# Performance work log

Hardware: AMD Instinct MI355X
Metric: run time of the kernel (lower is better)

The kernel has to match this reference:

```python
import jax, jax.numpy as jnp
import numpy as np

D, H, DH, DF = 128, 8, 16, 512
N_Q, N_KV, E = 20000, 20000, 640000


def _xavier(key, shape):
    fan_in, fan_out = shape[1], shape[0]
    lim = float(np.sqrt(6.0 / (fan_in + fan_out)))
    return jax.random.uniform(key, shape, jnp.float32, -lim, lim)


def layer_norm(x, g, b, eps=1e-5):
    mu = jnp.mean(x, axis=-1, keepdims=True)
    var = jnp.var(x, axis=-1, keepdims=True)
    return (x - mu) * jax.lax.rsqrt(var + eps) * g + b


def setup_inputs() -> dict:
    key = jax.random.key(0)
    ks = jax.random.split(key, 12)
    return {
        "q_feat": jax.random.normal(ks[0], (N_Q, D), jnp.float32),
        "kv_feat": jax.random.normal(ks[1], (N_KV, D), jnp.float32),
        "src": jax.random.randint(ks[2], (E,), 0, N_KV, jnp.int32),
        "dst": jax.random.randint(ks[3], (E,), 0, N_Q, jnp.int32),
        "Wq": _xavier(ks[4], (H * DH, D)),
        "Wk": _xavier(ks[5], (H * DH, D)),
        "Wv": _xavier(ks[6], (H * DH, D)),
        "Wo": _xavier(ks[7], (D, H * DH)),
        "W1": _xavier(ks[8], (DF, D)),
        "bf1": jnp.zeros((DF,), jnp.float32),
        "W2": _xavier(ks[9], (D, DF)),
        "bf2": jnp.zeros((D,), jnp.float32),
        "ln1_g": jnp.ones((D,), jnp.float32),
        "ln1_b": jnp.zeros((D,), jnp.float32),
        "ln2_g": jnp.ones((D,), jnp.float32),
        "ln2_b": jnp.zeros((D,), jnp.float32),
    }


def reference(q_feat, kv_feat, src, dst, Wq, Wk, Wv, Wo, W1, bf1, W2, bf2,
              ln1_g, ln1_b, ln2_g, ln2_b):
    n_q = q_feat.shape[0]
    # projections -> [N, H, DH]
    q = (q_feat @ Wq.T).reshape(-1, H, DH)
    k = (kv_feat @ Wk.T).reshape(-1, H, DH)
    v = (kv_feat @ Wv.T).reshape(-1, H, DH)
    # edge scores: u_mul_v then sum over d_head, scaled (score per edge per head)
    score = jnp.einsum('ehd,ehd->eh', k[src], q[dst]) / np.sqrt(DH)
    # edge_softmax grouped by destination node
    mx = jax.ops.segment_max(score, dst, num_segments=n_q)  # [Nq, H]
    ex = jnp.exp(score - mx[dst])
    denom = jax.ops.segment_sum(ex, dst, num_segments=n_q)
    att = ex / denom[dst]  # [E, H]
    # weighted scatter-sum of values to destination nodes
    msg = v[src] * att[:, :, None]  # [E, H, DH]
    out = jax.ops.segment_sum(msg, dst, num_segments=n_q)  # [Nq, H, DH]
    sa = out.reshape(n_q, H * DH) @ Wo.T
    feat = layer_norm(q_feat + sa, ln1_g, ln1_b)
    ff = jax.nn.relu(feat @ W1.T + bf1) @ W2.T + bf2
    return layer_norm(feat + ff, ln2_g, ln2_b)
```

## Files before the change

kernel.cpp:

```cpp
#include <hip/hip_runtime.h>
#include <hip/hip_fp16.h>
#include <math.h>
#include <type_traits>

#define D 128
#define NH 8
#define DHD 16
#define DF 512
#define STR 128

typedef _Float16 half8 __attribute__((ext_vector_type(8)));
typedef _Float16 half4 __attribute__((ext_vector_type(4)));
typedef float f32x4 __attribute__((ext_vector_type(4)));


__global__ __launch_bounds__(256) void mega_kernel(
    const float* __restrict__ q_feat, const float* __restrict__ kv_feat,
    const float* __restrict__ Wq, const float* __restrict__ Wk,
    const float* __restrict__ Wv,
    __half* __restrict__ fq, __half* __restrict__ fkv, int NQ, int NKV,
    const int* __restrict__ dst, const int* __restrict__ src,
    int* __restrict__ cnt, int* __restrict__ srcg, int E,
    const float* __restrict__ Wo, const float* __restrict__ W1,
    const float* __restrict__ W2,
    __half* __restrict__ wo16, __half* __restrict__ w116, __half* __restrict__ w216) {
    __shared__ __align__(16) __half As[128 * 128];
    __shared__ __align__(16) __half Ws[64 * 128];

    int xt = blockIdx.x;
    int tid = threadIdx.x;

    if (xt >= 2) {
        if (xt == 18) {
            int g = blockIdx.y * 256 + tid;
            if (g < 36864) {
                const float* s;
                __half* d;
                int idx = g;
                if (idx < 4096) { s = Wo; d = wo16; }
                else if (idx < 20480) { idx -= 4096; s = W1; d = w116; }
                else { idx -= 20480; s = W2; d = w216; }
                float4 f = ((const float4*)s)[idx];
                ushort4 o;
                o.x = __half_as_ushort(__float2half(f.x));
                o.y = __half_as_ushort(__float2half(f.y));
                o.z = __half_as_ushort(__float2half(f.z));
                o.w = __half_as_ushort(__float2half(f.w));
                ((ushort4*)d)[idx] = o;
            }
            return;
        }
        int b = (xt - 2) * gridDim.y + blockIdx.y;
        int i = b * 256 + tid;
        if (i < E) {
            int dn = dst[i];
            int p = atomicAdd(&cnt[dn], 1);
            if (p < STR) srcg[((size_t)dn << 7) + p] = src[i];
        }
        return;
    }

    const float* A = xt ? kv_feat : q_feat;
    __half* C = xt ? fkv : fq;
    int O = xt ? 256 : 128;
    int NCT = xt ? 4 : 2;
    int N = xt ? NKV : NQ;
    int row0 = blockIdx.y * 128;
    if (row0 >= N) return;

    int lane = tid & 63;
    int w = tid >> 6;
    int wm = w >> 1, wn = w & 1;
    int l16 = lane & 15, lq = lane >> 4;

#pragma unroll
    for (int i = 0; i < 8; ++i) {
        int f = tid + i * 256;
        int ln = f & 63;
        int mt = (f >> 6) & 7;
        int kc = f >> 9;
        int m = row0 + mt * 16 + (ln & 15);
        int k = kc * 32 + (ln >> 4) * 8;
        half8 v = {};
        if (m < N) {
            const float4* p = (const float4*)(A + (size_t)m * 128 + k);
            float4 f0 = p[0], f1 = p[1];
            v = (half8){(_Float16)f0.x, (_Float16)f0.y, (_Float16)f0.z, (_Float16)f0.w,
                        (_Float16)f1.x, (_Float16)f1.y, (_Float16)f1.z, (_Float16)f1.w};
        }
        ((half8*)As)[f] = v;
    }

    for (int ct = 0; ct < NCT; ++ct) {
        __syncthreads();
#pragma unroll
        for (int i = 0; i < 4; ++i) {
            int f = tid + i * 256;
            int ln = f & 63;
            int nt = (f >> 6) & 3;
            int kc = f >> 8;
            int n = ct * 64 + nt * 16 + (ln & 15);
            int k = kc * 32 + (ln >> 4) * 8;
            const float* Wsrc;
            int r;
            if (xt == 0) {
                Wsrc = Wq; r = n;
            } else {
                int h = n >> 5, qd = (n >> 3) & 3, isv = (n >> 2) & 1, d2 = n & 3;
                r = h * 16 + qd * 4 + d2;
                Wsrc = isv ? Wv : Wk;
            }
            const float4* p = (const float4*)(Wsrc + (size_t)r * 128 + k);
            float4 f0 = p[0], f1 = p[1];
            ((half8*)Ws)[f] = (half8){(_Float16)f0.x, (_Float16)f0.y, (_Float16)f0.z, (_Float16)f0.w,
                                      (_Float16)f1.x, (_Float16)f1.y, (_Float16)f1.z, (_Float16)f1.w};
        }
        __syncthreads();
        f32x4 acc[4][2];
#pragma unroll
        for (int i = 0; i < 4; ++i)
#pragma unroll
            for (int j = 0; j < 2; ++j) acc[i][j] = (f32x4){0.f, 0.f, 0.f, 0.f};
#pragma unroll
        for (int kc = 0; kc < 4; ++kc) {
            half8 a[4], b[2];
#pragma unroll
            for (int i = 0; i < 4; ++i) a[i] = ((half8*)As)[(kc * 8 + wm * 4 + i) * 64 + lane];
#pragma unroll
            for (int j = 0; j < 2; ++j) b[j] = ((half8*)Ws)[(kc * 4 + wn * 2 + j) * 64 + lane];
#pragma unroll
            for (int i = 0; i < 4; ++i)
#pragma unroll
                for (int j = 0; j < 2; ++j)
                    acc[i][j] = __builtin_amdgcn_mfma_f32_16x16x32_f16(a[i], b[j], acc[i][j], 0, 0, 0);
        }
#pragma unroll
        for (int i = 0; i < 4; ++i) {
            int rbase = row0 + (wm * 4 + i) * 16 + lq * 4;
#pragma unroll
            for (int j = 0; j < 2; ++j) {
                int c = ct * 64 + (wn * 2 + j) * 16 + l16;
#pragma unroll
                for (int r = 0; r < 4; ++r) {
                    int row = rbase + r;
                    if (row < N) C[(size_t)row * O + c] = __float2half(acc[i][j][r]);
                }
            }
        }
    }
}


__global__ __launch_bounds__(256) void attn_kernel(
    const __half* __restrict__ q, const __half* __restrict__ kv,
    const int* __restrict__ srcg, const int* __restrict__ cnt,
    __half* __restrict__ out, int NQ) {
    int n = blockIdx.x * 4 + (threadIdx.x >> 6);
    if (n >= NQ) return;
    int lane = threadIdx.x & 63;
    int eh = lane >> 5;
    int sub = lane & 31;
    int doff = sub << 2;
    half4 q4 = *(const half4*)(q + (size_t)n * D + doff);
    float q0 = (float)q4[0] * 0.25f, q1 = (float)q4[1] * 0.25f;
    float q2 = (float)q4[2] * 0.25f, q3 = (float)q4[3] * 0.25f;
    int s0 = n << 7;
    int c_ = cnt[n];
    int s1 = s0 + (c_ < STR ? c_ : STR);
    float lA = 0.f, lB = 0.f, lC = 0.f, lD = 0.f;
    f32x4 aA = {0.f, 0.f, 0.f, 0.f}, aB = {0.f, 0.f, 0.f, 0.f};
    f32x4 aC = {0.f, 0.f, 0.f, 0.f}, aD = {0.f, 0.f, 0.f, 0.f};
    int j = s0;
    for (; j + 8 <= s1; j += 8) {
        int e0 = srcg[j + eh];
        int e1 = srcg[j + 2 + eh];
        int e2 = srcg[j + 4 + eh];
        int e3 = srcg[j + 6 + eh];
        half8 c0 = *(const half8*)(kv + (size_t)e0 * 256 + (sub << 3));
        half8 c1 = *(const half8*)(kv + (size_t)e1 * 256 + (sub << 3));
        half8 c2 = *(const half8*)(kv + (size_t)e2 * 256 + (sub << 3));
        half8 c3 = *(const half8*)(kv + (size_t)e3 * 256 + (sub << 3));
        float p0 = q0 * (float)c0[0] + q1 * (float)c0[1] + q2 * (float)c0[2] + q3 * (float)c0[3];
        float p1 = q0 * (float)c1[0] + q1 * (float)c1[1] + q2 * (float)c1[2] + q3 * (float)c1[3];
        float p2 = q0 * (float)c2[0] + q1 * (float)c2[1] + q2 * (float)c2[2] + q3 * (float)c2[3];
        float p3 = q0 * (float)c3[0] + q1 * (float)c3[1] + q2 * (float)c3[2] + q3 * (float)c3[3];
        p0 += __shfl_xor(p0, 1, 4); p0 += __shfl_xor(p0, 2, 4);
        p1 += __shfl_xor(p1, 1, 4); p1 += __shfl_xor(p1, 2, 4);
        p2 += __shfl_xor(p2, 1, 4); p2 += __shfl_xor(p2, 2, 4);
        p3 += __shfl_xor(p3, 1, 4); p3 += __shfl_xor(p3, 2, 4);
        float x0 = __expf(fminf(p0, 70.f));
        float x1 = __expf(fminf(p1, 70.f));
        float x2 = __expf(fminf(p2, 70.f));
        float x3 = __expf(fminf(p3, 70.f));
        lA += x0; lB += x1; lC += x2; lD += x3;
        aA[0] += x0 * (float)c0[4]; aA[1] += x0 * (float)c0[5];
        aA[2] += x0 * (float)c0[6]; aA[3] += x0 * (float)c0[7];
        aB[0] += x1 * (float)c1[4]; aB[1] += x1 * (float)c1[5];
        aB[2] += x1 * (float)c1[6]; aB[3] += x1 * (float)c1[7];
        aC[0] += x2 * (float)c2[4]; aC[1] += x2 * (float)c2[5];
        aC[2] += x2 * (float)c2[6]; aC[3] += x2 * (float)c2[7];
        aD[0] += x3 * (float)c3[4]; aD[1] += x3 * (float)c3[5];
        aD[2] += x3 * (float)c3[6]; aD[3] += x3 * (float)c3[7];
    }
    for (; j + 4 <= s1; j += 4) {
        int e0 = srcg[j + eh];
        int e1 = srcg[j + 2 + eh];
        half8 c0 = *(const half8*)(kv + (size_t)e0 * 256 + (sub << 3));
        half8 c1 = *(const half8*)(kv + (size_t)e1 * 256 + (sub << 3));
        float p0 = q0 * (float)c0[0] + q1 * (float)c0[1] + q2 * (float)c0[2] + q3 * (float)c0[3];
        float p1 = q0 * (float)c1[0] + q1 * (float)c1[1] + q2 * (float)c1[2] + q3 * (float)c1[3];
        p0 += __shfl_xor(p0, 1, 4); p0 += __shfl_xor(p0, 2, 4);
        p1 += __shfl_xor(p1, 1, 4); p1 += __shfl_xor(p1, 2, 4);
        float x0 = __expf(fminf(p0, 70.f));
        float x1 = __expf(fminf(p1, 70.f));
        lA += x0; lB += x1;
        aA[0] += x0 * (float)c0[4]; aA[1] += x0 * (float)c0[5];
        aA[2] += x0 * (float)c0[6]; aA[3] += x0 * (float)c0[7];
        aB[0] += x1 * (float)c1[4]; aB[1] += x1 * (float)c1[5];
        aB[2] += x1 * (float)c1[6]; aB[3] += x1 * (float)c1[7];
    }
    for (; j < s1; j += 2) {
        bool valid = (j + eh) < s1;
        int e0 = srcg[valid ? (j + eh) : s0];
        half8 c0 = *(const half8*)(kv + (size_t)e0 * 256 + (sub << 3));
        float p0 = q0 * (float)c0[0] + q1 * (float)c0[1] + q2 * (float)c0[2] + q3 * (float)c0[3];
        p0 += __shfl_xor(p0, 1, 4); p0 += __shfl_xor(p0, 2, 4);
        float x0 = valid ? __expf(fminf(p0, 70.f)) : 0.f;
        lA += x0;
        aA[0] += x0 * (float)c0[4]; aA[1] += x0 * (float)c0[5];
        aA[2] += x0 * (float)c0[6]; aA[3] += x0 * (float)c0[7];
    }
    float l = (lA + lB) + (lC + lD);
    f32x4 a;
#pragma unroll
    for (int i = 0; i < 4; ++i) a[i] = (aA[i] + aB[i]) + (aC[i] + aD[i]);
    l += __shfl_xor(l, 32);
#pragma unroll
    for (int i = 0; i < 4; ++i) a[i] += __shfl_xor(a[i], 32);
    if (eh == 0) {
        float rl = (l > 0.f) ? 1.f / l : 0.f;
        half4 o = {(_Float16)(a[0] * rl), (_Float16)(a[1] * rl),
                   (_Float16)(a[2] * rl), (_Float16)(a[3] * rl)};
        *(half4*)(out + (size_t)n * D + doff) = o;
    }
}


__device__ __forceinline__ int feat_idx64(int rr, int mt, int c) {
    return (((c >> 5) * 4 + mt) * 64 + ((c >> 3) & 3) * 16 + rr) * 8 + (c & 7);
}

__global__ __launch_bounds__(256) void tail_kernel(
    const __half* __restrict__ A , const __half* __restrict__ Wo16,
    const float* __restrict__ res1 ,
    const float* __restrict__ g1, const float* __restrict__ b1,
    const __half* __restrict__ W1h, const float* __restrict__ fb1,
    const __half* __restrict__ W2h, const float* __restrict__ fb2,
    const float* __restrict__ g2, const float* __restrict__ b2,
    float* __restrict__ out, int N) {
    __shared__ __align__(16) __half Feat[64 * 128];
    __shared__ __align__(16) __half S1[64 * 128];
    __shared__ __align__(16) __half S2[128 * 64];
    __shared__ __align__(16) __half Hs[64 * 64];
    int tid = threadIdx.x, lane = tid & 63, w = tid >> 6;
    int row0 = blockIdx.x * 64;
    int l16 = lane & 15, lq = lane >> 4;

#pragma unroll
    for (int i = 0; i < 4; ++i) {
        int f = tid + i * 256;
        int ln = f & 63, mt = (f >> 6) & 3, kc = f >> 8;
        int m = row0 + mt * 16 + (ln & 15);
        int k = kc * 32 + (ln >> 4) * 8;
        half8 av = {};
        if (m < N) av = *(const half8*)(A + (size_t)m * D + k);
        ((half8*)S1)[f] = av;
    }

    f32x4 acc[8];
#pragma unroll
    for (int j = 0; j < 8; ++j) acc[j] = (f32x4){0.f, 0.f, 0.f, 0.f};
#pragma unroll
    for (int kt = 0; kt < 2; ++kt) {
        __syncthreads();
#pragma unroll
        for (int i = 0; i < 4; ++i) {
            int f = tid + i * 256;
            int ln = f & 63, ot = (f >> 6) & 7, kc2 = f >> 9;
            int o = ot * 16 + (ln & 15);
            int k = kt * 64 + kc2 * 32 + (ln >> 4) * 8;
            ((half8*)S2)[f] = *(const half8*)(Wo16 + (size_t)o * D + k);
        }
        __syncthreads();
#pragma unroll
        for (int kc2 = 0; kc2 < 2; ++kc2) {
            half8 a = ((half8*)S1)[((kt * 2 + kc2) * 4 + w) * 64 + lane];
            half8 bf[8];
#pragma unroll
            for (int j = 0; j < 8; ++j) bf[j] = ((half8*)S2)[(kc2 * 8 + j) * 64 + lane];
#pragma unroll
            for (int j = 0; j < 8; ++j)
                acc[j] = __builtin_amdgcn_mfma_f32_16x16x32_f16(a, bf[j], acc[j], 0, 0, 0);
        }
    }
    __syncthreads();

#pragma unroll
    for (int r = 0; r < 4; ++r) {
        int rr = lq * 4 + r;
        int row = row0 + w * 16 + rr;
        bool valid = row < N;
        float vals[8];
        float s = 0.f, sq = 0.f;
#pragma unroll
        for (int j = 0; j < 8; ++j) {
            int c = j * 16 + l16;
            float v = acc[j][r];
            if (valid) v += res1[(size_t)row * D + c];
            vals[j] = v;
            s += v;
            sq += v * v;
        }
#pragma unroll
        for (int m = 1; m < 16; m <<= 1) {
            s += __shfl_xor(s, m, 16);
            sq += __shfl_xor(sq, m, 16);
        }
        float mu = s * (1.f / 128.f);
        float var = sq * (1.f / 128.f) - mu * mu;
        float inv = rsqrtf(var + 1e-5f);
#pragma unroll
        for (int j = 0; j < 8; ++j) {
            int c = j * 16 + l16;
            float o = (vals[j] - mu) * inv * g1[c] + b1[c];
            Feat[feat_idx64(rr, w, c)] = __float2half(o);
        }
    }
    __syncthreads();

    half8 a_all[4];
#pragma unroll
    for (int kc = 0; kc < 4; ++kc)
        a_all[kc] = ((half8*)Feat)[(kc * 4 + w) * 64 + lane];

    f32x4 oacc[8];
#pragma unroll
    for (int j = 0; j < 8; ++j) oacc[j] = (f32x4){0.f, 0.f, 0.f, 0.f};

    for (int hc = 0; hc < 8; ++hc) {
        __syncthreads();
#pragma unroll
        for (int i = 0; i < 4; ++i) {
            int f = tid + i * 256;
            int ln = f & 63, nt = (f >> 6) & 3, kc = f >> 8;
            int n = hc * 64 + nt * 16 + (ln & 15);
            int k = kc * 32 + (ln >> 4) * 8;
            ((half8*)S1)[f] = *(const half8*)(W1h + (size_t)n * D + k);
        }
#pragma unroll
        for (int i = 0; i < 4; ++i) {
            int f = tid + i * 256;
            int ln = f & 63, ot = (f >> 6) & 7, kc2 = f >> 9;
            int o = ot * 16 + (ln & 15);
            int k = hc * 64 + kc2 * 32 + (ln >> 4) * 8;
            ((half8*)S2)[f] = *(const half8*)(W2h + (size_t)o * DF + k);
        }
        __syncthreads();
        f32x4 hacc[4];
#pragma unroll
        for (int j = 0; j < 4; ++j) hacc[j] = (f32x4){0.f, 0.f, 0.f, 0.f};
#pragma unroll
        for (int kc = 0; kc < 4; ++kc) {
            half8 b[4];
#pragma unroll
            for (int j = 0; j < 4; ++j) b[j] = ((half8*)S1)[(kc * 4 + j) * 64 + lane];
#pragma unroll
            for (int j = 0; j < 4; ++j)
                hacc[j] = __builtin_amdgcn_mfma_f32_16x16x32_f16(a_all[kc], b[j], hacc[j], 0, 0, 0);
        }
#pragma unroll
        for (int j = 0; j < 4; ++j) {
            float bias1 = fb1[hc * 64 + j * 16 + l16];
#pragma unroll
            for (int r = 0; r < 4; ++r) {
                float v = fmaxf(hacc[j][r] + bias1, 0.f);
                int kc2 = j >> 1;
                int lanep = ((j & 1) * 2 + (l16 >> 3)) * 16 + lq * 4 + r;
                Hs[((kc2 * 4 + w) * 64 + lanep) * 8 + (l16 & 7)] = __float2half(v);
            }
        }
        __syncthreads();
#pragma unroll
        for (int kc2 = 0; kc2 < 2; ++kc2) {
            half8 a = ((half8*)Hs)[(kc2 * 4 + w) * 64 + lane];
            half8 b[8];
#pragma unroll
            for (int ot = 0; ot < 8; ++ot) b[ot] = ((half8*)S2)[(kc2 * 8 + ot) * 64 + lane];
#pragma unroll
            for (int ot = 0; ot < 8; ++ot)
                oacc[ot] = __builtin_amdgcn_mfma_f32_16x16x32_f16(a, b[ot], oacc[ot], 0, 0, 0);
        }
    }

#pragma unroll
    for (int r = 0; r < 4; ++r) {
        int rr = lq * 4 + r;
        int row = row0 + w * 16 + rr;
        bool valid = row < N;
        float vals[8];
        float s = 0.f, sq = 0.f;
#pragma unroll
        for (int j = 0; j < 8; ++j) {
            int c = j * 16 + l16;
            float v = oacc[j][r] + fb2[c] + __half2float(Feat[feat_idx64(rr, w, c)]);
            vals[j] = v;
            s += v;
            sq += v * v;
        }
#pragma unroll
        for (int m = 1; m < 16; m <<= 1) {
            s += __shfl_xor(s, m, 16);
            sq += __shfl_xor(sq, m, 16);
        }
        float mu = s * (1.f / 128.f);
        float var = sq * (1.f / 128.f) - mu * mu;
        float inv = rsqrtf(var + 1e-5f);
        if (valid) {
#pragma unroll
            for (int j = 0; j < 8; ++j) {
                int c = j * 16 + l16;
                out[(size_t)row * D + c] = (vals[j] - mu) * inv * g2[c] + b2[c];
            }
        }
    }
}


extern "C" void kernel_launch(void* const* d_in, const int* in_sizes, int n_in,
                              void* d_out, int out_size, void* d_ws, size_t ws_size,
                              hipStream_t stream) {
    const float* q_feat = (const float*)d_in[0];
    const float* kv_feat = (const float*)d_in[1];
    const int* src = (const int*)d_in[2];
    const int* dst = (const int*)d_in[3];
    const float* Wq = (const float*)d_in[4];
    const float* Wk = (const float*)d_in[5];
    const float* Wv = (const float*)d_in[6];
    const float* Wo = (const float*)d_in[7];
    const float* W1 = (const float*)d_in[8];
    const float* bf1 = (const float*)d_in[9];
    const float* W2 = (const float*)d_in[10];
    const float* bf2 = (const float*)d_in[11];
    const float* ln1g = (const float*)d_in[12];
    const float* ln1b = (const float*)d_in[13];
    const float* ln2g = (const float*)d_in[14];
    const float* ln2b = (const float*)d_in[15];

    int NQ = in_sizes[0] / D;
    int NKV = in_sizes[1] / D;
    int E = in_sizes[2];
    float* out = (float*)d_out;

    char* base = (char*)d_ws;
    size_t off = 0;
    auto alloc = [&](size_t bytes) -> void* {
        void* p = base + off;
        off += (bytes + 255) & ~(size_t)255;
        return p;
    };
    __half* fq16 = (__half*)alloc((size_t)NQ * D * 2);
    __half* fkv = (__half*)alloc((size_t)NKV * 256 * 2);
    __half* fattn16 = (__half*)alloc((size_t)NQ * D * 2);
    int* cnt = (int*)alloc((size_t)NQ * 4);
    int* srcg = (int*)alloc((size_t)NQ * STR * 4);
    __half* wo16 = (__half*)alloc((size_t)D * D * 2);
    __half* w116 = (__half*)alloc((size_t)DF * D * 2);
    __half* w216 = (__half*)alloc((size_t)D * DF * 2);

    hipMemsetAsync(cnt, 0, (size_t)NQ * sizeof(int), stream);

    dim3 blk(256);
    int NMX = NQ > NKV ? NQ : NKV;
    int ytiles = (NMX + 127) / 128;
    mega_kernel<<<dim3(19, ytiles), blk, 0, stream>>>(
        q_feat, kv_feat, Wq, Wk, Wv, fq16, fkv, NQ, NKV,
        dst, src, cnt, srcg, E, Wo, W1, W2, wo16, w116, w216);

    attn_kernel<<<(NQ + 3) / 4, blk, 0, stream>>>(fq16, fkv, srcg, cnt, fattn16, NQ);

    tail_kernel<<<(NQ + 63) / 64, blk, 0, stream>>>(
        fattn16, wo16, q_feat, ln1g, ln1b, w116, bf1, w216, bf2, ln2g, ln2b, out, NQ);
}
```

Baseline: 215.9 us.

## Shrink projection tiles, vectorize CSR fill, store 16-bit source indices

Narrows the projection GEMM row tile from 128 to 64 rows, with each wave covering 16 rows across all 64 columns. This doubles the block count and halves shared memory per block, aiming for better occupancy. The edge bucketing now handles four edges per thread with int4 loads and stores source indices as 16-bit values, halving the srcg footprint and its traffic. The 16-bit indices assume NKV fits in 65536, and the grid is resized to match.

After: 213.1 us. About the same (-1.3%).

```diff
diff --git a/kernel.cpp b/kernel.cpp
--- a/kernel.cpp
+++ b/kernel.cpp
@@ -20,18 +20,18 @@
     const float* __restrict__ Wv,
     __half* __restrict__ fq, __half* __restrict__ fkv, int NQ, int NKV,
     const int* __restrict__ dst, const int* __restrict__ src,
-    int* __restrict__ cnt, int* __restrict__ srcg, int E,
+    int* __restrict__ cnt, unsigned short* __restrict__ srcg, int E,
     const float* __restrict__ Wo, const float* __restrict__ W1,
     const float* __restrict__ W2,
     __half* __restrict__ wo16, __half* __restrict__ w116, __half* __restrict__ w216) {
-    __shared__ __align__(16) __half As[128 * 128];
+    __shared__ __align__(16) __half As[64 * 128];
     __shared__ __align__(16) __half Ws[64 * 128];
 
     int xt = blockIdx.x;
     int tid = threadIdx.x;
 
     if (xt >= 2) {
-        if (xt == 18) {
+        if (xt == (int)gridDim.x - 1) {
             int g = blockIdx.y * 256 + tid;
             if (g < 36864) {
                 const float* s;
@@ -51,11 +51,28 @@
             return;
         }
         int b = (xt - 2) * gridDim.y + blockIdx.y;
-        int i = b * 256 + tid;
-        if (i < E) {
-            int dn = dst[i];
-            int p = atomicAdd(&cnt[dn], 1);
-            if (p < STR) srcg[((size_t)dn << 7) + p] = src[i];
+        int i4 = b * 256 + tid;
+        int base = i4 << 2;
+        if (base < E) {
+            int dd[4], ss[4];
+            if (base + 3 < E) {
+                int4 d4 = ((const int4*)dst)[i4];
+                int4 s4 = ((const int4*)src)[i4];
+                dd[0] = d4.x; dd[1] = d4.y; dd[2] = d4.z; dd[3] = d4.w;
+                ss[0] = s4.x; ss[1] = s4.y; ss[2] = s4.z; ss[3] = s4.w;
+#pragma unroll
+                for (int u = 0; u < 4; ++u) {
+                    int p = atomicAdd(&cnt[dd[u]], 1);
+                    if (p < STR) srcg[((size_t)dd[u] << 7) + p] = (unsigned short)ss[u];
+                }
+            } else {
+                for (int u = 0; u < 4 && base + u < E; ++u) {
+                    int dn = dst[base + u];
+                    int sn = src[base + u];
+                    int p = atomicAdd(&cnt[dn], 1);
+                    if (p < STR) srcg[((size_t)dn << 7) + p] = (unsigned short)sn;
+                }
+            }
         }
         return;
     }
@@ -65,20 +82,19 @@
     int O = xt ? 256 : 128;
     int NCT = xt ? 4 : 2;
     int N = xt ? NKV : NQ;
-    int row0 = blockIdx.y * 128;
+    int row0 = blockIdx.y * 64;
     if (row0 >= N) return;
 
     int lane = tid & 63;
     int w = tid >> 6;
-    int wm = w >> 1, wn = w & 1;
     int l16 = lane & 15, lq = lane >> 4;
 
 #pragma unroll
-    for (int i = 0; i < 8; ++i) {
+    for (int i = 0; i < 4; ++i) {
         int f = tid + i * 256;
         int ln = f & 63;
-        int mt = (f >> 6) & 7;
-        int kc = f >> 9;
+        int mt = (f >> 6) & 3;
+        int kc = f >> 8;
         int m = row0 + mt * 16 + (ln & 15);
         int k = kc * 32 + (ln >> 4) * 8;
         half8 v = {};
@@ -116,35 +132,26 @@
                                       (_Float16)f1.x, (_Float16)f1.y, (_Float16)f1.z, (_Float16)f1.w};
         }
         __syncthreads();
-        f32x4 acc[4][2];
-#pragma unroll
-        for (int i = 0; i < 4; ++i)
-#pragma unroll
-            for (int j = 0; j < 2; ++j) acc[i][j] = (f32x4){0.f, 0.f, 0.f, 0.f};
+        f32x4 acc[4];
+#pragma unroll
+        for (int j = 0; j < 4; ++j) acc[j] = (f32x4){0.f, 0.f, 0.f, 0.f};
 #pragma unroll
         for (int kc = 0; kc < 4; ++kc) {
-            half8 a[4], b[2];
-#pragma unroll
-            for (int i = 0; i < 4; ++i) a[i] = ((half8*)As)[(kc * 8 + wm * 4 + i) * 64 + lane];
-#pragma unroll
-            for (int j = 0; j < 2; ++j) b[j] = ((half8*)Ws)[(kc * 4 + wn * 2 + j) * 64 + lane];
-#pragma unroll
-            for (int i = 0; i < 4; ++i)
-#pragma unroll
-                for (int j = 0; j < 2; ++j)
-                    acc[i][j] = __builtin_amdgcn_mfma_f32_16x16x32_f16(a[i], b[j], acc[i][j], 0, 0, 0);
-        }
-#pragma unroll
-        for (int i = 0; i < 4; ++i) {
-            int rbase = row0 + (wm * 4 + i) * 16 + lq * 4;
-#pragma unroll
-            for (int j = 0; j < 2; ++j) {
-                int c = ct * 64 + (wn * 2 + j) * 16 + l16;
-#pragma unroll
-                for (int r = 0; r < 4; ++r) {
-                    int row = rbase + r;
-                    if (row < N) C[(size_t)row * O + c] = __float2half(acc[i][j][r]);
-                }
+            half8 a = ((half8*)As)[(kc * 4 + w) * 64 + lane];
+            half8 b[4];
+#pragma unroll
+            for (int j = 0; j < 4; ++j) b[j] = ((half8*)Ws)[(kc * 4 + j) * 64 + lane];
+#pragma unroll
+            for (int j = 0; j < 4; ++j)
+                acc[j] = __builtin_amdgcn_mfma_f32_16x16x32_f16(a, b[j], acc[j], 0, 0, 0);
+        }
+#pragma unroll
+        for (int j = 0; j < 4; ++j) {
+            int c = ct * 64 + j * 16 + l16;
+#pragma unroll
+            for (int r = 0; r < 4; ++r) {
+                int row = row0 + w * 16 + lq * 4 + r;
+                if (row < N) C[(size_t)row * O + c] = __float2half(acc[j][r]);
             }
         }
     }
@@ -153,7 +160,7 @@
 
 __global__ __launch_bounds__(256) void attn_kernel(
     const __half* __restrict__ q, const __half* __restrict__ kv,
-    const int* __restrict__ srcg, const int* __restrict__ cnt,
+    const unsigned short* __restrict__ srcg, const int* __restrict__ cnt,
     __half* __restrict__ out, int NQ) {
     int n = blockIdx.x * 4 + (threadIdx.x >> 6);
     if (n >= NQ) return;
@@ -472,7 +479,7 @@
     __half* fkv = (__half*)alloc((size_t)NKV * 256 * 2);
     __half* fattn16 = (__half*)alloc((size_t)NQ * D * 2);
     int* cnt = (int*)alloc((size_t)NQ * 4);
-    int* srcg = (int*)alloc((size_t)NQ * STR * 4);
+    unsigned short* srcg = (unsigned short*)alloc((size_t)NQ * STR * 2);
     __half* wo16 = (__half*)alloc((size_t)D * D * 2);
     __half* w116 = (__half*)alloc((size_t)DF * D * 2);
     __half* w216 = (__half*)alloc((size_t)D * DF * 2);
@@ -481,8 +488,10 @@
 
     dim3 blk(256);
     int NMX = NQ > NKV ? NQ : NKV;
-    int ytiles = (NMX + 127) / 128;
-    mega_kernel<<<dim3(19, ytiles), blk, 0, stream>>>(
+    int ytiles = (NMX + 63) / 64;
+    int fillBlocks = (E + 1023) / 1024;
+    int fillPlanes = (fillBlocks + ytiles - 1) / ytiles;
+    mega_kernel<<<dim3(3 + fillPlanes, ytiles), blk, 0, stream>>>(
         q_feat, kv_feat, Wq, Wk, Wv, fq16, fkv, NQ, NKV,
         dst, src, cnt, srcg, E, Wo, W1, W2, wo16, w116, w216);
 
```
